# Kernel optimization log

Hardware: AMD Instinct MI355X
Metric: run time of the kernel (lower is better)

## Reference

```python
import jax, jax.numpy as jnp
import numpy as np

W = 512  # imgSize
B = 32

def setup_inputs() -> dict:
    key = jax.random.key(0)
    input_diffgrid = jax.random.normal(key, (B, 2, W, W), dtype=jnp.float32)
    return {"input_diffgrid": input_diffgrid}

def reference(input_diffgrid) -> jnp.ndarray:
    # conv_transpose2d with ones kernel (1,1,1,W) then crop [0:W] along width
    # == cumulative sum along width; likewise (1,1,W,1) == cumsum along height.
    x = jnp.cumsum(input_diffgrid[:, 0], axis=-1)  # [B, W, W], cumsum over width
    y = jnp.cumsum(input_diffgrid[:, 1], axis=-2)  # [B, W, W], cumsum over height
    return jnp.stack((x, y), axis=1)  # [B, 2, W, W]
```

## Files before the change

### kernel.cpp

```cpp
#include <hip/hip_runtime.h>

#define IMG_W 512
#define NB 32

__device__ __forceinline__ void row_cumsum_wave(const float* __restrict__ in,
                                                float* __restrict__ out,
                                                int gwave) {
    const int lane = threadIdx.x & 63;
    const int b = gwave >> 9;
    const int row = gwave & 511;
    const long base = ((long)(b * 2 + 0) * IMG_W + row) * IMG_W;

    const float4 va = *reinterpret_cast<const float4*>(in + base + lane * 4);
    const float4 vb = *reinterpret_cast<const float4*>(in + base + 256 + lane * 4);

    const float a0 = va.x, a1 = a0 + va.y, a2 = a1 + va.z, a3 = a2 + va.w;
    const float b0 = vb.x, b1 = b0 + vb.y, b2 = b1 + vb.z, b3 = b2 + vb.w;

    float ta = a3, tb = b3;
#pragma unroll
    for (int d = 1; d < 64; d <<= 1) {
        const float ua = __shfl_up(ta, d);
        const float ub = __shfl_up(tb, d);
        if (lane >= d) { ta += ua; tb += ub; }
    }
    const float totalA = __shfl(ta, 63);
    const float exA = ta - a3;
    const float exB = totalA + (tb - b3);

    float4 oa, ob;
    oa.x = exA + a0; oa.y = exA + a1; oa.z = exA + a2; oa.w = exA + a3;
    ob.x = exB + b0; ob.y = exB + b1; ob.z = exB + b2; ob.w = exB + b3;
    *reinterpret_cast<float4*>(out + base + lane * 4) = oa;
    *reinterpret_cast<float4*>(out + base + 256 + lane * 4) = ob;
}


template <int S>
__global__ __launch_bounds__(256) void k1_fused(const float* __restrict__ in,
                                                float* __restrict__ out,
                                                float* __restrict__ ws,
                                                int yblocksA) {
    constexpr int ROWS = IMG_W / S;
    if ((int)blockIdx.x < yblocksA) {
        const int yb = blockIdx.x;
        const int b = yb / (S / 2);
        const int sp = yb % (S / 2);
        const int s = sp * 2 + (threadIdx.x >> 7);
        const int grp = threadIdx.x & 127;
        const long ibase = ((long)(b * 2 + 1) * IMG_W + (long)s * ROWS) * IMG_W + grp * 4;
        float4 acc = make_float4(0.f, 0.f, 0.f, 0.f);
#pragma unroll
        for (int r = 0; r < ROWS; ++r) {
            const float4 v = *reinterpret_cast<const float4*>(in + ibase + (long)r * IMG_W);
            acc.x += v.x; acc.y += v.y; acc.z += v.z; acc.w += v.w;
        }
        *reinterpret_cast<float4*>(ws + ((long)b * S + s) * IMG_W + grp * 4) = acc;
    } else {
        const int gwave = (blockIdx.x - yblocksA) * 4 + (threadIdx.x >> 6);
        row_cumsum_wave(in, out, gwave);
    }
}

template <int S>
__global__ __launch_bounds__(128) void k2_scan(const float* __restrict__ in,
                                               float* __restrict__ out,
                                               const float* __restrict__ ws) {
    constexpr int ROWS = IMG_W / S;
    const int yb = blockIdx.x;
    const int b = yb / S;
    const int s = yb % S;
    const int grp = threadIdx.x;

    float4 acc = make_float4(0.f, 0.f, 0.f, 0.f);
    for (int u = 0; u < s; ++u) {
        const float4 w = *reinterpret_cast<const float4*>(ws + ((long)b * S + u) * IMG_W + grp * 4);
        acc.x += w.x; acc.y += w.y; acc.z += w.z; acc.w += w.w;
    }

    const long ibase = ((long)(b * 2 + 1) * IMG_W + (long)s * ROWS) * IMG_W + grp * 4;
#pragma unroll
    for (int r = 0; r < ROWS; ++r) {
        const float4 v = *reinterpret_cast<const float4*>(in + ibase + (long)r * IMG_W);
        acc.x += v.x; acc.y += v.y; acc.z += v.z; acc.w += v.w;
        *reinterpret_cast<float4*>(out + ibase + (long)r * IMG_W) = acc;
    }
}

template <int S>
static void launch_impl(const float* in, float* out, float* ws, hipStream_t stream) {
    const int yblocksA = NB * (S / 2);
    const int xblocks = (NB * IMG_W) / 4;
    k1_fused<S><<<yblocksA + xblocks, 256, 0, stream>>>(in, out, ws, yblocksA);
    k2_scan<S><<<NB * S, 128, 0, stream>>>(in, out, ws);
}

extern "C" void kernel_launch(void* const* d_in, const int* in_sizes, int n_in,
                              void* d_out, int out_size, void* d_ws, size_t ws_size,
                              hipStream_t stream) {
    const float* in = (const float*)d_in[0];
    float* out = (float*)d_out;
    float* ws = (float*)d_ws;

    const size_t per_seg = (size_t)NB * IMG_W * sizeof(float);
    if (ws_size >= 32 * per_seg)      launch_impl<32>(in, out, ws, stream);
    else if (ws_size >= 16 * per_seg) launch_impl<16>(in, out, ws, stream);
    else                              launch_impl<8>(in, out, ws, stream);
}
```

Measured before the change: 119.2 us.

## Fuse column scan into single kernel using LDS-staged full-height column tiles

Replaces the two-kernel scheme (partial segment sums to a workspace, then a second scan pass) with one kernel. Each column block loads a full 512x64 column strip into LDS, does segmented scans plus an offset pass inside the block, and writes the result, so the y channel is read once and the workspace round trip and second launch go away. Row-scan waves share the same launch with 1024-thread blocks. The cost is about 136KB of LDS per block, which limits occupancy to one column block per CU, and only 256 such blocks, with three block-wide barriers.

```diff
diff --git a/kernel.cpp b/kernel.cpp
--- a/kernel.cpp
+++ b/kernel.cpp
@@ -2,6 +2,15 @@
 
 #define IMG_W 512
 #define NB 32
+
+#define YBLOCKS (NB * 8)
+#define XBLOCKS 1024
+#define THREADS 1024
+#define SEGS 16
+#define ROWSEG 32
+#define COLS 64
+#define TILE_FLOATS (IMG_W * COLS)
+#define LDS_FLOATS (TILE_FLOATS + 2 * SEGS * COLS)
 
 __device__ __forceinline__ void row_cumsum_wave(const float* __restrict__ in,
                                                 float* __restrict__ out,
@@ -35,64 +44,63 @@
     *reinterpret_cast<float4*>(out + base + 256 + lane * 4) = ob;
 }
 
+extern "C" __global__ __launch_bounds__(THREADS)
+void gsi_fused(const float* __restrict__ in, float* __restrict__ out) {
+    extern __shared__ float lds[];
+    const int tid = threadIdx.x;
 
-template <int S>
-__global__ __launch_bounds__(256) void k1_fused(const float* __restrict__ in,
-                                                float* __restrict__ out,
-                                                float* __restrict__ ws,
-                                                int yblocksA) {
-    constexpr int ROWS = IMG_W / S;
-    if ((int)blockIdx.x < yblocksA) {
-        const int yb = blockIdx.x;
-        const int b = yb / (S / 2);
-        const int sp = yb % (S / 2);
-        const int s = sp * 2 + (threadIdx.x >> 7);
-        const int grp = threadIdx.x & 127;
-        const long ibase = ((long)(b * 2 + 1) * IMG_W + (long)s * ROWS) * IMG_W + grp * 4;
-        float4 acc = make_float4(0.f, 0.f, 0.f, 0.f);
+    if ((int)blockIdx.x < YBLOCKS) {
+        float* tot = lds + TILE_FLOATS;
+        float* off = tot + SEGS * COLS;
+        const int b = blockIdx.x >> 3;
+        const int colg = blockIdx.x & 7;
+        const long ybase = ((long)(b * 2 + 1) * IMG_W) * IMG_W + colg * COLS;
+
 #pragma unroll
-        for (int r = 0; r < ROWS; ++r) {
-            const float4 v = *reinterpret_cast<const float4*>(in + ibase + (long)r * IMG_W);
-            acc.x += v.x; acc.y += v.y; acc.z += v.z; acc.w += v.w;
+        for (int it = 0; it < 8; ++it) {
+            const int idx = it * THREADS + tid;
+            const int row = idx >> 4;
+            const int c4 = idx & 15;
+            const float4 v = *reinterpret_cast<const float4*>(
+                in + ybase + (long)row * IMG_W + c4 * 4);
+            *reinterpret_cast<float4*>(lds + row * COLS + c4 * 4) = v;
         }
-        *reinterpret_cast<float4*>(ws + ((long)b * S + s) * IMG_W + grp * 4) = acc;
+        __syncthreads();
+
+        const int col = tid & 63;
+        const int seg = tid >> 6;
+        const int rbase = seg * ROWSEG;
+        float acc = 0.f;
+#pragma unroll
+        for (int r = 0; r < ROWSEG; ++r) {
+            const int a = (rbase + r) * COLS + col;
+            acc += lds[a];
+            lds[a] = acc;
+        }
+        tot[seg * COLS + col] = acc;
+        __syncthreads();
+
+        float o = 0.f;
+        for (int u = 0; u < seg; ++u) o += tot[u * COLS + col];
+        off[seg * COLS + col] = o;
+        __syncthreads();
+
+#pragma unroll
+        for (int it = 0; it < 8; ++it) {
+            const int idx = it * THREADS + tid;
+            const int row = idx >> 4;
+            const int c4 = idx & 15;
+            const int sg = row >> 5;
+            const float4 v = *reinterpret_cast<const float4*>(lds + row * COLS + c4 * 4);
+            const float4 o4 = *reinterpret_cast<const float4*>(off + sg * COLS + c4 * 4);
+            float4 w;
+            w.x = v.x + o4.x; w.y = v.y + o4.y; w.z = v.z + o4.z; w.w = v.w + o4.w;
+            *reinterpret_cast<float4*>(out + ybase + (long)row * IMG_W + c4 * 4) = w;
+        }
     } else {
-        const int gwave = (blockIdx.x - yblocksA) * 4 + (threadIdx.x >> 6);
+        const int gwave = ((int)blockIdx.x - YBLOCKS) * 16 + (tid >> 6);
         row_cumsum_wave(in, out, gwave);
     }
-}
-
-template <int S>
-__global__ __launch_bounds__(128) void k2_scan(const float* __restrict__ in,
-                                               float* __restrict__ out,
-                                               const float* __restrict__ ws) {
-    constexpr int ROWS = IMG_W / S;
-    const int yb = blockIdx.x;
-    const int b = yb / S;
-    const int s = yb % S;
-    const int grp = threadIdx.x;
-
-    float4 acc = make_float4(0.f, 0.f, 0.f, 0.f);
-    for (int u = 0; u < s; ++u) {
-        const float4 w = *reinterpret_cast<const float4*>(ws + ((long)b * S + u) * IMG_W + grp * 4);
-        acc.x += w.x; acc.y += w.y; acc.z += w.z; acc.w += w.w;
-    }
-
-    const long ibase = ((long)(b * 2 + 1) * IMG_W + (long)s * ROWS) * IMG_W + grp * 4;
-#pragma unroll
-    for (int r = 0; r < ROWS; ++r) {
-        const float4 v = *reinterpret_cast<const float4*>(in + ibase + (long)r * IMG_W);
-        acc.x += v.x; acc.y += v.y; acc.z += v.z; acc.w += v.w;
-        *reinterpret_cast<float4*>(out + ibase + (long)r * IMG_W) = acc;
-    }
-}
-
-template <int S>
-static void launch_impl(const float* in, float* out, float* ws, hipStream_t stream) {
-    const int yblocksA = NB * (S / 2);
-    const int xblocks = (NB * IMG_W) / 4;
-    k1_fused<S><<<yblocksA + xblocks, 256, 0, stream>>>(in, out, ws, yblocksA);
-    k2_scan<S><<<NB * S, 128, 0, stream>>>(in, out, ws);
 }
 
 extern "C" void kernel_launch(void* const* d_in, const int* in_sizes, int n_in,
@@ -100,10 +108,9 @@
                               hipStream_t stream) {
     const float* in = (const float*)d_in[0];
     float* out = (float*)d_out;
-    float* ws = (float*)d_ws;
+    const int lds_bytes = LDS_FLOATS * 4;
 
-    const size_t per_seg = (size_t)NB * IMG_W * sizeof(float);
-    if (ws_size >= 32 * per_seg)      launch_impl<32>(in, out, ws, stream);
-    else if (ws_size >= 16 * per_seg) launch_impl<16>(in, out, ws, stream);
-    else                              launch_impl<8>(in, out, ws, stream);
+    (void)hipFuncSetAttribute(reinterpret_cast<const void*>(gsi_fused),
+                              hipFuncAttributeMaxDynamicSharedMemorySize, lds_bytes);
+    gsi_fused<<<YBLOCKS + XBLOCKS, THREADS, lds_bytes, stream>>>(in, out);
 }
```

Result: faster. 111.2 us (-6.7%).
